# Kernel optimization log

Measured on AMD Instinct MI355X. Metric: run time of the kernel, lower is better.

The kernel has to match this reference:

```python
import jax, jax.numpy as jnp
import numpy as np

B, T, DKQ, DV, EKQ, EV, H, OUT = 8, 2048, 64, 64, 128, 128, 4, 32
FF = 4 * EV
NEG = -1e30  # additive mask value (safe stand-in for -inf)


def _ln(x, g, b, eps=1e-5):
    m = x.mean(-1, keepdims=True)
    var = ((x - m) ** 2).mean(-1, keepdims=True)
    return (x - m) * jax.lax.rsqrt(var + eps) * g + b


def _attn(q, k, v, mask):
    # q,k,v: [n, T, E] -> heads [n, H, T, dh]; NOTE: no 1/sqrt(d) scaling (faithful to source)
    n, t, _ = q.shape
    q = q.reshape(n, t, H, -1).transpose(0, 2, 1, 3)
    k = k.reshape(n, t, H, -1).transpose(0, 2, 1, 3)
    v = v.reshape(n, t, H, -1).transpose(0, 2, 1, 3)
    w = jnp.einsum('bhqd,bhkd->bhqk', q, k) + mask  # [n,H,T,T]
    a = jax.nn.softmax(w, axis=-1)
    o = jnp.einsum('bhqk,bhkd->bhqd', a, v)
    return o.transpose(0, 2, 1, 3).reshape(n, t, -1)


def setup_inputs() -> dict:
    key = jax.random.key(0)
    ks = jax.random.split(key, 32)
    w = lambda k, s: jax.random.normal(k, s, jnp.float32) * 0.02
    DIN_A = DKQ + DV
    return {
        'kq': jax.random.normal(ks[0], (B, T, DKQ), jnp.float32),
        'v': jax.random.normal(ks[1], (B, T, DV), jnp.float32),
        # Layer A (input_dim = DKQ+DV, embed = EV)
        'A_Wk': w(ks[2], (DIN_A, EV)), 'A_bk': jnp.zeros((EV,), jnp.float32),
        'A_Wq': w(ks[3], (DIN_A, EV)), 'A_bq': jnp.zeros((EV,), jnp.float32),
        'A_Wv': w(ks[4], (DIN_A, EV)), 'A_bv': jnp.zeros((EV,), jnp.float32),
        'A_f1W': w(ks[5], (EV, FF)), 'A_f1b': jnp.zeros((FF,), jnp.float32),
        'A_f2W': w(ks[6], (FF, EV)), 'A_f2b': jnp.zeros((EV,), jnp.float32),
        'A_n1g': jnp.ones((EV,), jnp.float32), 'A_n1b': jnp.zeros((EV,), jnp.float32),
        'A_n2g': jnp.ones((EV,), jnp.float32), 'A_n2b': jnp.zeros((EV,), jnp.float32),
        # Layer B (kq -> EKQ, vA -> EV)
        'B_Wk': w(ks[7], (DKQ, EKQ)), 'B_bk': jnp.zeros((EKQ,), jnp.float32),
        'B_Wq': w(ks[8], (DKQ, EKQ)), 'B_bq': jnp.zeros((EKQ,), jnp.float32),
        'B_Wv': w(ks[9], (EV, EV)), 'B_bv': jnp.zeros((EV,), jnp.float32),
        'B_f1W': w(ks[10], (EV, FF)), 'B_f1b': jnp.zeros((FF,), jnp.float32),
        'B_f2W': w(ks[11], (FF, EV)), 'B_f2b': jnp.zeros((EV,), jnp.float32),
        # Output head
        'out_W': w(ks[12], (EV, OUT)), 'out_b': jnp.zeros((OUT,), jnp.float32),
    }


def reference(kq, v, A_Wk, A_bk, A_Wq, A_bq, A_Wv, A_bv, A_f1W, A_f1b, A_f2W, A_f2b,
              A_n1g, A_n1b, A_n2g, A_n2b, B_Wk, B_bk, B_Wq, B_bq, B_Wv, B_bv,
              B_f1W, B_f1b, B_f2W, B_f2b, out_W, out_b):
    n, t, _ = kq.shape
    i = jnp.arange(t)[:, None]
    j = jnp.arange(t)[None, :]
    mask_a = jnp.where(j <= i, 0.0, NEG).astype(jnp.float32)               # causal (diag=1)
    mask_b = jnp.where((j < i) | ((i == 0) & (j == 0)), 0.0, NEG).astype(jnp.float32)  # strict causal + (0,0) exception

    # ---- Layer A ----
    X = jnp.concatenate([kq, v], axis=-1)
    K = X @ A_Wk + A_bk
    Q = X @ A_Wq + A_bq
    V = X @ A_Wv + A_bv
    attn_out = _attn(Q, K, V, mask_a)
    h1 = _ln(V + attn_out, A_n1g, A_n1b)
    ff = jax.nn.gelu(h1 @ A_f1W + A_f1b, approximate=False) @ A_f2W + A_f2b
    vA = _ln(h1 + ff, A_n2g, A_n2b)

    # ---- Layer B (no residuals / norms: values is overwritten in source) ----
    K2 = kq @ B_Wk + B_bk
    Q2 = kq @ B_Wq + B_bq
    V2 = vA @ B_Wv + B_bv
    attn_out2 = _attn(Q2, K2, V2, mask_b)
    ff2 = jax.nn.gelu(attn_out2 @ B_f1W + B_f1b, approximate=False) @ B_f2W + B_f2b

    return ff2 @ out_W + out_b
```

## Files before the change

kernel.cpp:

```cpp
#include <hip/hip_runtime.h>
#include <hip/hip_bf16.h>

#define TSEQ 2048
#define NBATCH 8
#define NROWS (NBATCH*TSEQ)
#define EMB 128
#define NH 4
#define DH 32
#define OUTD 32
#define APLANE (NROWS*EMB)

typedef short s8v __attribute__((ext_vector_type(8)));
typedef float f4v __attribute__((ext_vector_type(4)));

__device__ __forceinline__ unsigned short f2bf(float f){
  unsigned int u = __float_as_uint(f);
  unsigned int r = u + 0x7fffu + ((u >> 16) & 1u);
  return (unsigned short)(r >> 16);
}
__device__ __forceinline__ float bf2f(unsigned short u){
  return __uint_as_float(((unsigned int)u) << 16);
}

struct WPack {
  const float* src[10];
  int off[10];
  int ntk[10];
  int rowoff[10];
  int nsh[10];
  int kn[10];
};
__global__ __launch_bounds__(256) void prep_w(WPack p, short* __restrict__ warena){
  int blk = blockIdx.x, m = 0;
  #pragma unroll
  for (int i=0;i<10;i++){
    int nb = p.kn[i] >> 8;
    if (blk < nb){ m = i; break; }
    blk -= nb;
  }
  int idx = blk*256 + threadIdx.x;
  float x = p.src[m][idx];
  int nsh = p.nsh[m];
  int n = idx & ((1<<nsh)-1);
  int k = idx >> nsh;
  int K = p.kn[m] >> nsh;
  unsigned short hi = f2bf(x);
  unsigned short lo = f2bf(x - bf2f(hi));
  short* dh = warena + p.off[m] + (size_t)(p.rowoff[m] + n)*K + k;
  dh[0]        = (short)hi;
  dh[p.ntk[m]] = (short)lo;
}

__global__ __launch_bounds__(256) void xsplit(const float* __restrict__ kq, const float* __restrict__ v,
                                              unsigned short* __restrict__ X){
  int idx = blockIdx.x*256 + threadIdx.x;
  int row = idx >> 7, c = idx & 127;
  float val = (c < 64) ? kq[row*64 + c] : v[row*64 + (c-64)];
  unsigned short hi = f2bf(val);
  X[idx]          = hi;
  X[idx + APLANE] = f2bf(val - bf2f(hi));
}

struct GOuts {
  const float* bias[3];
  float* of[3];
  unsigned short* ob[3];
};
__global__ __launch_bounds__(256) void gemm2(
    const unsigned short* __restrict__ A, int aplane, int lda, int K, int niter,
    const short* __restrict__ wt, int NTK,
    GOuts og, int NT, int nseg, int act){
  __shared__ short As[2][2][64*40];
  const int tid  = threadIdx.x;
  const int w    = tid >> 6;
  const int lane = tid & 63;
  const int col  = lane & 15;
  const int quad = lane >> 4;
  const int row0 = blockIdx.x * 64;
  const int colg = blockIdx.y*64 + w*16 + col;
  const bool two = (aplane != 0);

  f4v acc[4];
  #pragma unroll
  for (int i=0;i<4;i++) acc[i] = (f4v){0.f,0.f,0.f,0.f};

  const int ar = tid >> 2, ac = (tid & 3)*8;
  const unsigned short* abase = A + (size_t)(row0 + ar)*lda;

  s8v pah, pal;
  pah = *(const s8v*)(abase + ac);
  if (two) pal = *(const s8v*)(abase + aplane + ac);

  for (int i=0;i<niter;i++){
    const int buf = i & 1;
    *(s8v*)&As[buf][0][ar*40 + ac] = pah;
    if (two) *(s8v*)&As[buf][1][ar*40 + ac] = pal;
    __syncthreads();
    if (i+1 < niter){
      const int kcol = (i+1)*32 + ac;
      pah = *(const s8v*)(abase + kcol);
      if (two) pal = *(const s8v*)(abase + aplane + kcol);
    }
    const short* wp = wt + (size_t)colg*K + i*32 + quad*8;
    s8v bh = *(const s8v*)wp;
    s8v bl = *(const s8v*)(wp + NTK);
    #pragma unroll
    for (int rt=0;rt<4;rt++){
      s8v ah = *(const s8v*)&As[buf][0][(rt*16 + col)*40 + quad*8];
      acc[rt] = __builtin_amdgcn_mfma_f32_16x16x32_bf16(ah, bh, acc[rt], 0, 0, 0);
      if (two){
        s8v al = *(const s8v*)&As[buf][1][(rt*16 + col)*40 + quad*8];
        acc[rt] = __builtin_amdgcn_mfma_f32_16x16x32_bf16(al, bh, acc[rt], 0, 0, 0);
      }
      acc[rt] = __builtin_amdgcn_mfma_f32_16x16x32_bf16(ah, bl, acc[rt], 0, 0, 0);
    }
  }

  int seg, lcol, ldc;
  if (nseg > 1){ seg = colg >> 7; lcol = colg & 127; ldc = 128; }
  else         { seg = 0; lcol = colg; ldc = NT; }
  const float bv = og.bias[seg][lcol];
  float* of = og.of[seg];
  unsigned short* ob = og.ob[seg];
  #pragma unroll
  for (int rt=0;rt<4;rt++){
    #pragma unroll
    for (int r=0;r<4;r++){
      const int row = row0 + rt*16 + quad*4 + r;
      float val = acc[rt][r] + bv;
      if (act == 1) val = 0.5f*val*(1.f + erff(val*0.70710678118654752440f));
      if (ob) ob[(size_t)row*ldc + lcol] = f2bf(val);
      else    of[(size_t)row*ldc + lcol] = val;
    }
  }
}

__global__ __launch_bounds__(256) void vtrans(const float* __restrict__ V, unsigned short* __restrict__ Vtb){
  __shared__ short Lt[64*40];
  const int tid = threadIdx.x;
  const int t0 = blockIdx.x * 64;
  const int bh = blockIdx.y;
  const int b = bh >> 2, h = bh & 3;
  {
    const int r = tid >> 2, c = (tid & 3)*8;
    const float* src = V + (size_t)(b*TSEQ + t0 + r)*EMB + h*DH + c;
    float4 x0 = *(const float4*)src;
    float4 x1 = *(const float4*)(src + 4);
    s8v kb;
    kb[0]=(short)f2bf(x0.x); kb[1]=(short)f2bf(x0.y); kb[2]=(short)f2bf(x0.z); kb[3]=(short)f2bf(x0.w);
    kb[4]=(short)f2bf(x1.x); kb[5]=(short)f2bf(x1.y); kb[6]=(short)f2bf(x1.z); kb[7]=(short)f2bf(x1.w);
    *(s8v*)&Lt[r*40 + c] = kb;
  }
  __syncthreads();
  const int d = tid >> 3, kc = (tid & 7)*8;
  s8v o;
  #pragma unroll
  for (int j=0;j<8;j++) o[j] = Lt[(kc + j)*40 + d];
  *(s8v*)(Vtb + ((size_t)bh*32 + d)*TSEQ + t0 + kc) = o;
}

#define KT_STRIDE 40
#define VT_STRIDE 72
#define PW_STRIDE 72
__global__ __launch_bounds__(128) void flash3(const unsigned short* __restrict__ Qb,
                                              const unsigned short* __restrict__ Kb,
                                              const unsigned short* __restrict__ Vtb,
                                              float* __restrict__ O0, float* __restrict__ O1,
                                              float* __restrict__ L0, float* __restrict__ L1,
                                              int mode){
  __shared__ short Kt[64*KT_STRIDE];
  __shared__ short Vt[32*VT_STRIDE];
  __shared__ short Pw[2][16*PW_STRIDE];
  const int tid  = threadIdx.x;
  const int w    = tid >> 6;
  const int lane = tid & 63;
  const int col  = lane & 15;
  const int quad = lane >> 4;
  const int bh = blockIdx.y;
  const int b = bh >> 2, h = bh & 3;
  const int par = blockIdx.z;
  float* Op = par ? O1 : O0;
  float* Lp = par ? L1 : L0;
  const int kr = tid >> 1, kc16 = (tid & 1)*16;
  const int vd = tid >> 2, vk16 = (tid & 3)*16;

  for (int pass = 0; pass < 2; pass++){
    const int t = pass ? blockIdx.x : (63 - blockIdx.x);
    const int qbase = t*32 + w*16;
    const int jtmax = t >> 1;

    s8v qf = *(const s8v*)(Qb + (size_t)(b*TSEQ + qbase + col)*EMB + h*DH + quad*8);
    f4v o0 = {0.f,0.f,0.f,0.f}, o1 = {0.f,0.f,0.f,0.f};
    float lr[4] = {0.f,0.f,0.f,0.f};

    if (par <= jtmax){
      s8v ka, kb2, va, vb;
      {
        const unsigned short* kp = Kb + (size_t)(b*TSEQ + par*64 + kr)*EMB + h*DH + kc16;
        ka = *(const s8v*)kp; kb2 = *(const s8v*)(kp + 8);
        const unsigned short* vp = Vtb + ((size_t)bh*32 + vd)*TSEQ + par*64 + vk16;
        va = *(const s8v*)vp; vb = *(const s8v*)(vp + 8);
      }
      for (int jt = par; jt <= jtmax; jt += 2){
        __syncthreads();
        *(s8v*)&Kt[kr*KT_STRIDE + kc16]     = ka;
        *(s8v*)&Kt[kr*KT_STRIDE + kc16 + 8] = kb2;
        *(s8v*)&Vt[vd*VT_STRIDE + vk16]     = va;
        *(s8v*)&Vt[vd*VT_STRIDE + vk16 + 8] = vb;
        __syncthreads();
        if (jt + 2 <= jtmax){
          const unsigned short* kp = Kb + (size_t)(b*TSEQ + (jt+2)*64 + kr)*EMB + h*DH + kc16;
          ka = *(const s8v*)kp; kb2 = *(const s8v*)(kp + 8);
          const unsigned short* vp = Vtb + ((size_t)bh*32 + vd)*TSEQ + (jt+2)*64 + vk16;
          va = *(const s8v*)vp; vb = *(const s8v*)(vp + 8);
        }
        f4v s[4];
        #pragma unroll
        for (int t4=0;t4<4;t4++){
          s8v kf = *(const s8v*)&Kt[(t4*16 + col)*KT_STRIDE + quad*8];
          f4v z = {0.f,0.f,0.f,0.f};
          s[t4] = __builtin_amdgcn_mfma_f32_16x16x32_bf16(qf, kf, z, 0, 0, 0);
        }
        if (jt == jtmax){
          const int j0 = jt*64;
          #pragma unroll
          for (int t4=0;t4<4;t4++){
            const int jg = j0 + t4*16 + col;
            #pragma unroll
            for (int r=0;r<4;r++){
              const int qg = qbase + quad*4 + r;
              const bool ok = (mode==0) ? (jg <= qg) : ((jg < qg) || (qg==0 && jg==0));
              s[t4][r] = ok ? s[t4][r] : -1e30f;
            }
          }
        }
        #pragma unroll
        for (int t4=0;t4<4;t4++){
          #pragma unroll
          for (int r=0;r<4;r++){
            float pv = __expf(s[t4][r]);
            s[t4][r] = pv;
            lr[r] += pv;
            Pw[w][(quad*4+r)*PW_STRIDE + t4*16 + col] = (short)f2bf(pv);
          }
        }
        #pragma unroll
        for (int kk=0;kk<2;kk++){
          s8v pf  = *(const s8v*)&Pw[w][col*PW_STRIDE + kk*32 + quad*8];
          s8v vf0 = *(const s8v*)&Vt[(col)*VT_STRIDE    + kk*32 + quad*8];
          s8v vf1 = *(const s8v*)&Vt[(16+col)*VT_STRIDE + kk*32 + quad*8];
          o0 = __builtin_amdgcn_mfma_f32_16x16x32_bf16(pf, vf0, o0, 0, 0, 0);
          o1 = __builtin_amdgcn_mfma_f32_16x16x32_bf16(pf, vf1, o1, 0, 0, 0);
        }
      }
    }
    float* obase = Op + (size_t)(b*TSEQ + qbase)*EMB + h*DH;
    #pragma unroll
    for (int r=0;r<4;r++){
      float l = lr[r];
      l += __shfl_xor(l,1); l += __shfl_xor(l,2);
      l += __shfl_xor(l,4); l += __shfl_xor(l,8);
      obase[(size_t)(quad*4+r)*EMB + col]      = o0[r];
      obase[(size_t)(quad*4+r)*EMB + 16 + col] = o1[r];
      if (col == 0) Lp[(size_t)(b*TSEQ + qbase + quad*4 + r)*NH + h] = l;
    }
  }
}

__global__ __launch_bounds__(64) void combine_ln(const float* __restrict__ O0, const float* __restrict__ O1,
                                                 const float* __restrict__ L0, const float* __restrict__ L1,
                                                 const float* __restrict__ Vf,
                                                 const float* __restrict__ g, const float* __restrict__ bt,
                                                 unsigned short* __restrict__ outp){
  const int row = blockIdx.x;
  const int tid = threadIdx.x;
  const size_t base = (size_t)row*EMB;
  const int h0 = tid >> 5, h1i = 2 + (tid >> 5);
  const float la = L0[(size_t)row*NH + h0] + L1[(size_t)row*NH + h0];
  const float lb = L0[(size_t)row*NH + h1i] + L1[(size_t)row*NH + h1i];
  float x0 = Vf[base+tid]    + (O0[base+tid]    + O1[base+tid])    / la;
  float x1 = Vf[base+tid+64] + (O0[base+tid+64] + O1[base+tid+64]) / lb;
  float s  = x0 + x1;
  float s2 = x0*x0 + x1*x1;
  #pragma unroll
  for (int off=1; off<64; off<<=1){
    s  += __shfl_xor(s,  off);
    s2 += __shfl_xor(s2, off);
  }
  float mean = s * (1.f/128.f);
  float var  = s2 * (1.f/128.f) - mean*mean;
  float rstd = rsqrtf(var + 1e-5f);
  float y0 = (x0-mean)*rstd*g[tid]    + bt[tid];
  float y1 = (x1-mean)*rstd*g[tid+64] + bt[tid+64];
  unsigned short h0b = f2bf(y0), h1b = f2bf(y1);
  outp[base+tid]             = h0b;
  outp[base+tid+64]          = h1b;
  outp[base+tid+APLANE]      = f2bf(y0 - bf2f(h0b));
  outp[base+tid+64+APLANE]   = f2bf(y1 - bf2f(h1b));
}

__global__ __launch_bounds__(64) void ln2(const unsigned short* __restrict__ Xp, const float* __restrict__ R,
                                          const float* __restrict__ g, const float* __restrict__ bt,
                                          unsigned short* __restrict__ outp){
  const int row = blockIdx.x;
  const int tid = threadIdx.x;
  const size_t base = (size_t)row*EMB;
  float x0 = bf2f(Xp[base+tid])    + bf2f(Xp[base+tid+APLANE])    + R[base+tid];
  float x1 = bf2f(Xp[base+tid+64]) + bf2f(Xp[base+tid+64+APLANE]) + R[base+tid+64];
  float s  = x0 + x1;
  float s2 = x0*x0 + x1*x1;
  #pragma unroll
  for (int off=1; off<64; off<<=1){
    s  += __shfl_xor(s,  off);
    s2 += __shfl_xor(s2, off);
  }
  float mean = s * (1.f/128.f);
  float var  = s2 * (1.f/128.f) - mean*mean;
  float rstd = rsqrtf(var + 1e-5f);
  float y0 = (x0-mean)*rstd*g[tid]    + bt[tid];
  float y1 = (x1-mean)*rstd*g[tid+64] + bt[tid+64];
  unsigned short h0b = f2bf(y0), h1b = f2bf(y1);
  outp[base+tid]             = h0b;
  outp[base+tid+64]          = h1b;
  outp[base+tid+APLANE]      = f2bf(y0 - bf2f(h0b));
  outp[base+tid+64+APLANE]   = f2bf(y1 - bf2f(h1b));
}

__global__ __launch_bounds__(256) void combine_b(const float* __restrict__ O0, const float* __restrict__ O1,
                                                 const float* __restrict__ L0, const float* __restrict__ L1,
                                                 unsigned short* __restrict__ outp){
  const int idx = blockIdx.x*256 + threadIdx.x;
  const int row = idx >> 7, c = idx & 127, h = c >> 5;
  const float l = L0[(size_t)row*NH + h] + L1[(size_t)row*NH + h];
  const float v = (O0[idx] + O1[idx]) / l;
  unsigned short hb = f2bf(v);
  outp[idx]          = hb;
  outp[idx + APLANE] = f2bf(v - bf2f(hb));
}

__global__ __launch_bounds__(256) void out_proj(const float* __restrict__ A,
                                                const float* __restrict__ W, const float* __restrict__ bb,
                                                float* __restrict__ out){
  __shared__ float As[8*128];
  __shared__ float Ws2[128*32];
  const int tid = threadIdx.x;
  const int row0 = blockIdx.x * 8;
  for (int idx = tid; idx < 8*128; idx += 256) As[idx] = A[(size_t)row0*128 + idx];
  for (int idx = tid; idx < 128*32; idx += 256) Ws2[idx] = W[idx];
  __syncthreads();
  const int r = tid >> 5, c = tid & 31;
  float acc = bb[c];
  #pragma unroll 8
  for (int k=0;k<128;k++) acc = fmaf(As[r*128 + k], Ws2[k*32 + c], acc);
  out[(size_t)(row0 + r)*OUTD + c] = acc;
}

extern "C" void kernel_launch(void* const* d_in, const int* in_sizes, int n_in,
                              void* d_out, int out_size, void* d_ws, size_t ws_size,
                              hipStream_t stream) {
  const float* kq    = (const float*)d_in[0];
  const float* v     = (const float*)d_in[1];
  const float* A_Wk  = (const float*)d_in[2];  const float* A_bk  = (const float*)d_in[3];
  const float* A_Wq  = (const float*)d_in[4];  const float* A_bq  = (const float*)d_in[5];
  const float* A_Wv  = (const float*)d_in[6];  const float* A_bv  = (const float*)d_in[7];
  const float* A_f1W = (const float*)d_in[8];  const float* A_f1b = (const float*)d_in[9];
  const float* A_f2W = (const float*)d_in[10]; const float* A_f2b = (const float*)d_in[11];
  const float* A_n1g = (const float*)d_in[12]; const float* A_n1b = (const float*)d_in[13];
  const float* A_n2g = (const float*)d_in[14]; const float* A_n2b = (const float*)d_in[15];
  const float* B_Wk  = (const float*)d_in[16]; const float* B_bk  = (const float*)d_in[17];
  const float* B_Wq  = (const float*)d_in[18]; const float* B_bq  = (const float*)d_in[19];
  const float* B_Wv  = (const float*)d_in[20]; const float* B_bv  = (const float*)d_in[21];
  const float* B_f1W = (const float*)d_in[22]; const float* B_f1b = (const float*)d_in[23];
  const float* B_f2W = (const float*)d_in[24]; const float* B_f2b = (const float*)d_in[25];
  const float* out_W = (const float*)d_in[26]; const float* out_b = (const float*)d_in[27];
  float* out = (float*)d_out;
  (void)in_sizes; (void)n_in; (void)out_size; (void)ws_size;

  char* ws = (char*)d_ws;
  const size_t MB = 1024*1024;
  short* warena = (short*)ws;
  unsigned short* Xs  = (unsigned short*)(ws + 2*MB);
  unsigned short* Qbf = (unsigned short*)(ws + 10*MB);
  unsigned short* Kbf = (unsigned short*)(ws + 14*MB);
  unsigned short* Vtb = (unsigned short*)(ws + 18*MB);
  float* Vf  = (float*)(ws + 22*MB);
  float* O0  = (float*)(ws + 30*MB);
  float* O1  = (float*)(ws + 38*MB);
  float* L0  = (float*)(ws + 46*MB);
  float* L1  = (float*)(ws + 47*MB);
  unsigned short* h1p = (unsigned short*)(ws + 48*MB);
  unsigned short* mid = (unsigned short*)(ws + 56*MB);
  float* ffo = (float*)(ws + 72*MB);
  unsigned short* vAp = (unsigned short*)(ws + 80*MB);

  WPack p;
  const float* srcs[10] = {A_Wq,A_Wk,A_Wv,A_f1W,A_f2W,B_Wq,B_Wk,B_Wv,B_f1W,B_f2W};
  int kn[10]     = {16384,16384,16384,65536,65536,8192,8192,16384,65536,65536};
  int nsh[10]    = {7,7,7,9,7,7,7,7,9,7};
  int off[10]    = {0,0,0,98304,229376,360448,360448,393216,425984,557056};
  int ntk[10]    = {49152,49152,49152,65536,65536,16384,16384,16384,65536,65536};
  int rowoff[10] = {0,128,256,0,0,0,128,0,0,0};
  int nblk = 0;
  for (int i=0;i<10;i++){
    p.src[i]=srcs[i]; p.kn[i]=kn[i]; p.nsh[i]=nsh[i];
    p.off[i]=off[i]; p.ntk[i]=ntk[i]; p.rowoff[i]=rowoff[i];
    nblk += kn[i] >> 8;
  }
  prep_w<<<nblk, 256, 0, stream>>>(p, warena);
  xsplit<<<NROWS*128/256, 256, 0, stream>>>(kq, v, Xs);

  GOuts oQKVA = {{A_bq,A_bk,A_bv},{nullptr,nullptr,Vf},{Qbf,Kbf,nullptr}};
  GOuts oF1A  = {{A_f1b,nullptr,nullptr},{nullptr,nullptr,nullptr},{mid,nullptr,nullptr}};
  GOuts oF2A  = {{A_f2b,nullptr,nullptr},{ffo,nullptr,nullptr},{nullptr,nullptr,nullptr}};
  GOuts oQKB  = {{B_bq,B_bk,nullptr},{nullptr,nullptr,nullptr},{Qbf,Kbf,nullptr}};
  GOuts oVB   = {{B_bv,nullptr,nullptr},{Vf,nullptr,nullptr},{nullptr,nullptr,nullptr}};
  GOuts oF1B  = {{B_f1b,nullptr,nullptr},{nullptr,nullptr,nullptr},{mid,nullptr,nullptr}};
  GOuts oF2B  = {{B_f2b,nullptr,nullptr},{ffo,nullptr,nullptr},{nullptr,nullptr,nullptr}};

  gemm2<<<dim3(256,6), 256, 0, stream>>>(Xs, APLANE, 128, 128, 4, warena + 0,      49152, oQKVA, 384, 3, 0);
  vtrans<<<dim3(32,32), 256, 0, stream>>>(Vf, Vtb);
  flash3<<<dim3(32,32,2), 128, 0, stream>>>(Qbf, Kbf, Vtb, O0, O1, L0, L1, 0);
  combine_ln<<<NROWS, 64, 0, stream>>>(O0, O1, L0, L1, Vf, A_n1g, A_n1b, h1p);
  gemm2<<<dim3(256,8), 256, 0, stream>>>(h1p, APLANE, 128, 128, 4, warena + 98304, 65536, oF1A, 512, 1, 1);
  gemm2<<<dim3(256,2), 256, 0, stream>>>(mid, 0,      512, 512, 16, warena + 229376, 65536, oF2A, 128, 1, 0);
  ln2<<<NROWS, 64, 0, stream>>>(h1p, ffo, A_n2g, A_n2b, vAp);

  gemm2<<<dim3(256,4), 256, 0, stream>>>(Xs, APLANE, 128, 64, 2,  warena + 360448, 16384, oQKB, 256, 2, 0);
  gemm2<<<dim3(256,2), 256, 0, stream>>>(vAp, APLANE, 128, 128, 4, warena + 393216, 16384, oVB, 128, 1, 0);
  vtrans<<<dim3(32,32), 256, 0, stream>>>(Vf, Vtb);
  flash3<<<dim3(32,32,2), 128, 0, stream>>>(Qbf, Kbf, Vtb, O0, O1, L0, L1, 1);
  combine_b<<<NROWS*128/256, 256, 0, stream>>>(O0, O1, L0, L1, h1p);
  gemm2<<<dim3(256,8), 256, 0, stream>>>(h1p, APLANE, 128, 128, 4, warena + 425984, 65536, oF1B, 512, 1, 1);
  gemm2<<<dim3(256,2), 256, 0, stream>>>(mid, 0,      512, 512, 16, warena + 557056, 65536, oF2B, 128, 1, 0);

  out_proj<<<NROWS/8, 256, 0, stream>>>(ffo, out_W, out_b, out);
}
```

Baseline: 313.5 us.

## Fold FFN2 into output head, fuse V transpose into GEMM, swap flash operands

Several changes at once. B_f2W and out_W are pre-multiplied into one 512x32 matrix, so the last FFN2 GEMM and the output projection become a single small kernel reading the bf16 GELU activations. The V-transpose kernels are removed because the QKV/V GEMM epilogue now writes the transposed bf16 V directly. Q is prescaled by log2e so flash uses exp2. The flash MFMA operands are swapped so results are laid out per query row, allowing vectorized stores and a simpler row-sum reduction. The GEMM also prefetches B fragments a step ahead. The weight folding changes rounding order, and out2 is a plain FMA loop over K=512 per output, which may be slower than the MFMA GEMM it replaces.

```diff
diff --git a/kernel.cpp b/kernel.cpp
--- a/kernel.cpp
+++ b/kernel.cpp
@@ -9,8 +9,10 @@
 #define DH 32
 #define OUTD 32
 #define APLANE (NROWS*EMB)
+#define LOG2E 1.4426950408889634f
 
 typedef short s8v __attribute__((ext_vector_type(8)));
+typedef short s4v __attribute__((ext_vector_type(4)));
 typedef float f4v __attribute__((ext_vector_type(4)));
 
 __device__ __forceinline__ unsigned short f2bf(float f){
@@ -51,6 +53,24 @@
   dh[p.ntk[m]] = (short)lo;
 }
 
+__global__ __launch_bounds__(256) void prep_wc(const float* __restrict__ f2W, const float* __restrict__ f2b,
+                                               const float* __restrict__ oW, const float* __restrict__ ob,
+                                               float* __restrict__ Wc, float* __restrict__ bc){
+  int idx = blockIdx.x*256 + threadIdx.x;
+  if (idx < 512*32){
+    int k = idx >> 5, n = idx & 31;
+    float s = 0.f;
+    #pragma unroll 4
+    for (int j=0;j<128;j++) s = fmaf(f2W[k*128+j], oW[j*32+n], s);
+    Wc[idx] = s;
+  } else if (idx < 512*32 + 32){
+    int n = idx - 512*32;
+    float s = ob[n];
+    for (int j=0;j<128;j++) s = fmaf(f2b[j], oW[j*32+n], s);
+    bc[n] = s;
+  }
+}
+
 __global__ __launch_bounds__(256) void xsplit(const float* __restrict__ kq, const float* __restrict__ v,
                                               unsigned short* __restrict__ X){
   int idx = blockIdx.x*256 + threadIdx.x;
@@ -65,6 +85,8 @@
   const float* bias[3];
   float* of[3];
   unsigned short* ob[3];
+  unsigned short* vt[3];
+  float scale[3];
 };
 __global__ __launch_bounds__(256) void gemm2(
     const unsigned short* __restrict__ A, int aplane, int lda, int K, int niter,
@@ -86,24 +108,27 @@
 
   const int ar = tid >> 2, ac = (tid & 3)*8;
   const unsigned short* abase = A + (size_t)(row0 + ar)*lda;
-
-  s8v pah, pal;
+  const short* wbase = wt + (size_t)colg*K + quad*8;
+
+  s8v pah, pal, pbh, pbl;
   pah = *(const s8v*)(abase + ac);
   if (two) pal = *(const s8v*)(abase + aplane + ac);
+  pbh = *(const s8v*)(wbase);
+  pbl = *(const s8v*)(wbase + NTK);
 
   for (int i=0;i<niter;i++){
     const int buf = i & 1;
     *(s8v*)&As[buf][0][ar*40 + ac] = pah;
     if (two) *(s8v*)&As[buf][1][ar*40 + ac] = pal;
     __syncthreads();
+    s8v bh = pbh, bl = pbl;
     if (i+1 < niter){
-      const int kcol = (i+1)*32 + ac;
-      pah = *(const s8v*)(abase + kcol);
-      if (two) pal = *(const s8v*)(abase + aplane + kcol);
-    }
-    const short* wp = wt + (size_t)colg*K + i*32 + quad*8;
-    s8v bh = *(const s8v*)wp;
-    s8v bl = *(const s8v*)(wp + NTK);
+      const int kcol = (i+1)*32;
+      pah = *(const s8v*)(abase + kcol + ac);
+      if (two) pal = *(const s8v*)(abase + aplane + kcol + ac);
+      pbh = *(const s8v*)(wbase + kcol);
+      pbl = *(const s8v*)(wbase + NTK + kcol);
+    }
     #pragma unroll
     for (int rt=0;rt<4;rt++){
       s8v ah = *(const s8v*)&As[buf][0][(rt*16 + col)*40 + quad*8];
@@ -120,43 +145,41 @@
   if (nseg > 1){ seg = colg >> 7; lcol = colg & 127; ldc = 128; }
   else         { seg = 0; lcol = colg; ldc = NT; }
   const float bv = og.bias[seg][lcol];
+  const float sc = og.scale[seg];
   float* of = og.of[seg];
   unsigned short* ob = og.ob[seg];
+  unsigned short* vtp = og.vt[seg];
+  float vals[4][4];
   #pragma unroll
   for (int rt=0;rt<4;rt++){
     #pragma unroll
     for (int r=0;r<4;r++){
-      const int row = row0 + rt*16 + quad*4 + r;
       float val = acc[rt][r] + bv;
       if (act == 1) val = 0.5f*val*(1.f + erff(val*0.70710678118654752440f));
-      if (ob) ob[(size_t)row*ldc + lcol] = f2bf(val);
-      else    of[(size_t)row*ldc + lcol] = val;
-    }
-  }
-}
-
-__global__ __launch_bounds__(256) void vtrans(const float* __restrict__ V, unsigned short* __restrict__ Vtb){
-  __shared__ short Lt[64*40];
-  const int tid = threadIdx.x;
-  const int t0 = blockIdx.x * 64;
-  const int bh = blockIdx.y;
-  const int b = bh >> 2, h = bh & 3;
-  {
-    const int r = tid >> 2, c = (tid & 3)*8;
-    const float* src = V + (size_t)(b*TSEQ + t0 + r)*EMB + h*DH + c;
-    float4 x0 = *(const float4*)src;
-    float4 x1 = *(const float4*)(src + 4);
-    s8v kb;
-    kb[0]=(short)f2bf(x0.x); kb[1]=(short)f2bf(x0.y); kb[2]=(short)f2bf(x0.z); kb[3]=(short)f2bf(x0.w);
-    kb[4]=(short)f2bf(x1.x); kb[5]=(short)f2bf(x1.y); kb[6]=(short)f2bf(x1.z); kb[7]=(short)f2bf(x1.w);
-    *(s8v*)&Lt[r*40 + c] = kb;
-  }
-  __syncthreads();
-  const int d = tid >> 3, kc = (tid & 7)*8;
-  s8v o;
-  #pragma unroll
-  for (int j=0;j<8;j++) o[j] = Lt[(kc + j)*40 + d];
-  *(s8v*)(Vtb + ((size_t)bh*32 + d)*TSEQ + t0 + kc) = o;
+      vals[rt][r] = val * sc;
+    }
+  }
+  #pragma unroll
+  for (int rt=0;rt<4;rt++){
+    const int row = row0 + rt*16 + quad*4;
+    #pragma unroll
+    for (int r=0;r<4;r++){
+      if (ob)      ob[(size_t)(row+r)*ldc + lcol] = f2bf(vals[rt][r]);
+      else if (of) of[(size_t)(row+r)*ldc + lcol] = vals[rt][r];
+    }
+  }
+  if (vtp){
+    const int hh = lcol >> 5, dd = lcol & 31;
+    const int bb = row0 >> 11;
+    unsigned short* vbase = vtp + ((size_t)(bb*NH + hh)*32 + dd)*TSEQ + (row0 & (TSEQ-1)) + quad*4;
+    #pragma unroll
+    for (int rt=0;rt<4;rt++){
+      s4v pk;
+      #pragma unroll
+      for (int r=0;r<4;r++) pk[r] = (short)f2bf(vals[rt][r]);
+      *(s4v*)(vbase + rt*16) = pk;
+    }
+  }
 }
 
 #define KT_STRIDE 40
@@ -188,10 +211,11 @@
     const int t = pass ? blockIdx.x : (63 - blockIdx.x);
     const int qbase = t*32 + w*16;
     const int jtmax = t >> 1;
-
-    s8v qf = *(const s8v*)(Qb + (size_t)(b*TSEQ + qbase + col)*EMB + h*DH + quad*8);
+    const int qg = qbase + col;
+
+    s8v qf = *(const s8v*)(Qb + (size_t)(b*TSEQ + qg)*EMB + h*DH + quad*8);
     f4v o0 = {0.f,0.f,0.f,0.f}, o1 = {0.f,0.f,0.f,0.f};
-    float lr[4] = {0.f,0.f,0.f,0.f};
+    float lsum = 0.f;
 
     if (par <= jtmax){
       s8v ka, kb2, va, vb;
@@ -219,16 +243,15 @@
         for (int t4=0;t4<4;t4++){
           s8v kf = *(const s8v*)&Kt[(t4*16 + col)*KT_STRIDE + quad*8];
           f4v z = {0.f,0.f,0.f,0.f};
-          s[t4] = __builtin_amdgcn_mfma_f32_16x16x32_bf16(qf, kf, z, 0, 0, 0);
+          s[t4] = __builtin_amdgcn_mfma_f32_16x16x32_bf16(kf, qf, z, 0, 0, 0);
         }
         if (jt == jtmax){
           const int j0 = jt*64;
           #pragma unroll
           for (int t4=0;t4<4;t4++){
-            const int jg = j0 + t4*16 + col;
             #pragma unroll
             for (int r=0;r<4;r++){
-              const int qg = qbase + quad*4 + r;
+              const int jg = j0 + t4*16 + quad*4 + r;
               const bool ok = (mode==0) ? (jg <= qg) : ((jg < qg) || (qg==0 && jg==0));
               s[t4][r] = ok ? s[t4][r] : -1e30f;
             }
@@ -236,34 +259,31 @@
         }
         #pragma unroll
         for (int t4=0;t4<4;t4++){
+          s4v pk;
           #pragma unroll
           for (int r=0;r<4;r++){
-            float pv = __expf(s[t4][r]);
-            s[t4][r] = pv;
-            lr[r] += pv;
-            Pw[w][(quad*4+r)*PW_STRIDE + t4*16 + col] = (short)f2bf(pv);
+            float pv = exp2f(s[t4][r]);
+            lsum += pv;
+            pk[r] = (short)f2bf(pv);
           }
+          *(s4v*)&Pw[w][col*PW_STRIDE + t4*16 + quad*4] = pk;
         }
         #pragma unroll
         for (int kk=0;kk<2;kk++){
           s8v pf  = *(const s8v*)&Pw[w][col*PW_STRIDE + kk*32 + quad*8];
           s8v vf0 = *(const s8v*)&Vt[(col)*VT_STRIDE    + kk*32 + quad*8];
           s8v vf1 = *(const s8v*)&Vt[(16+col)*VT_STRIDE + kk*32 + quad*8];
-          o0 = __builtin_amdgcn_mfma_f32_16x16x32_bf16(pf, vf0, o0, 0, 0, 0);
-          o1 = __builtin_amdgcn_mfma_f32_16x16x32_bf16(pf, vf1, o1, 0, 0, 0);
+          o0 = __builtin_amdgcn_mfma_f32_16x16x32_bf16(vf0, pf, o0, 0, 0, 0);
+          o1 = __builtin_amdgcn_mfma_f32_16x16x32_bf16(vf1, pf, o1, 0, 0, 0);
         }
       }
     }
-    float* obase = Op + (size_t)(b*TSEQ + qbase)*EMB + h*DH;
-    #pragma unroll
-    for (int r=0;r<4;r++){
-      float l = lr[r];
-      l += __shfl_xor(l,1); l += __shfl_xor(l,2);
-      l += __shfl_xor(l,4); l += __shfl_xor(l,8);
-      obase[(size_t)(quad*4+r)*EMB + col]      = o0[r];
-      obase[(size_t)(quad*4+r)*EMB + 16 + col] = o1[r];
-      if (col == 0) Lp[(size_t)(b*TSEQ + qbase + quad*4 + r)*NH + h] = l;
-    }
+    lsum += __shfl_xor(lsum, 16);
+    lsum += __shfl_xor(lsum, 32);
+    float* obase = Op + (size_t)(b*TSEQ + qg)*EMB + h*DH + quad*4;
+    *(float4*)(obase)      = make_float4(o0[0],o0[1],o0[2],o0[3]);
+    *(float4*)(obase + 16) = make_float4(o1[0],o1[1],o1[2],o1[3]);
+    if (quad == 0) Lp[(size_t)(b*TSEQ + qg)*NH + h] = lsum;
   }
 }
 
@@ -338,21 +358,21 @@
   outp[idx + APLANE] = f2bf(v - bf2f(hb));
 }
 
-__global__ __launch_bounds__(256) void out_proj(const float* __restrict__ A,
-                                                const float* __restrict__ W, const float* __restrict__ bb,
-                                                float* __restrict__ out){
-  __shared__ float As[8*128];
-  __shared__ float Ws2[128*32];
+__global__ __launch_bounds__(256) void out2(const unsigned short* __restrict__ mid,
+                                            const float* __restrict__ Wc, const float* __restrict__ bc,
+                                            float* __restrict__ out){
+  __shared__ float As[8*512];
   const int tid = threadIdx.x;
-  const int row0 = blockIdx.x * 8;
-  for (int idx = tid; idx < 8*128; idx += 256) As[idx] = A[(size_t)row0*128 + idx];
-  for (int idx = tid; idx < 128*32; idx += 256) Ws2[idx] = W[idx];
+  const int row0 = blockIdx.x*8;
+  for (int idx = tid; idx < 8*512; idx += 256)
+    As[idx] = bf2f(mid[(size_t)row0*512 + idx]);
   __syncthreads();
   const int r = tid >> 5, c = tid & 31;
-  float acc = bb[c];
+  float acc = bc[c];
+  const float* as = &As[r*512];
   #pragma unroll 8
-  for (int k=0;k<128;k++) acc = fmaf(As[r*128 + k], Ws2[k*32 + c], acc);
-  out[(size_t)(row0 + r)*OUTD + c] = acc;
+  for (int k=0;k<512;k++) acc = fmaf(as[k], Wc[k*32+c], acc);
+  out[(size_t)(row0+r)*OUTD + c] = acc;
 }
 
 extern "C" void kernel_launch(void* const* d_in, const int* in_sizes, int n_in,
@@ -379,6 +399,8 @@
   char* ws = (char*)d_ws;
   const size_t MB = 1024*1024;
   short* warena = (short*)ws;
+  float* Wc  = (float*)(ws + 1536*1024);
+  float* bc  = (float*)(ws + 1536*1024 + 65536);
   unsigned short* Xs  = (unsigned short*)(ws + 2*MB);
   unsigned short* Qbf = (unsigned short*)(ws + 10*MB);
   unsigned short* Kbf = (unsigned short*)(ws + 14*MB);
@@ -407,18 +429,17 @@
     nblk += kn[i] >> 8;
   }
   prep_w<<<nblk, 256, 0, stream>>>(p, warena);
+  prep_wc<<<65, 256, 0, stream>>>(B_f2W, B_f2b, out_W, out_b, Wc, bc);
   xsplit<<<NROWS*128/256, 256, 0, stream>>>(kq, v, Xs);
 
-  GOuts oQKVA = {{A_bq,A_bk,A_bv},{nullptr,nullptr,Vf},{Qbf,Kbf,nullptr}};
-  GOuts oF1A  = {{A_f1b,nullptr,nullptr},{nullptr,nullptr,nullptr},{mid,nullptr,nullptr}};
-  GOuts oF2A  = {{A_f2b,nullptr,nullptr},{ffo,nullptr,nullptr},{nullptr,nullptr,nullptr}};
-  GOuts oQKB  = {{B_bq,B_bk,nullptr},{nullptr,nullptr,nullptr},{Qbf,Kbf,nullptr}};
-  GOuts oVB   = {{B_bv,nullptr,nullptr},{Vf,nullptr,nullptr},{nullptr,nullptr,nullptr}};
-  GOuts oF1B  = {{B_f1b,nullptr,nullptr},{nullptr,nullptr,nullptr},{mid,nullptr,nullptr}};
-  GOuts oF2B  = {{B_f2b,nullptr,nullptr},{ffo,nullptr,nullptr},{nullptr,nullptr,nullptr}};
+  GOuts oQKVA = {{A_bq,A_bk,A_bv},{nullptr,nullptr,Vf},{Qbf,Kbf,nullptr},{nullptr,nullptr,Vtb},{LOG2E,1.f,1.f}};
+  GOuts oF1A  = {{A_f1b,nullptr,nullptr},{nullptr,nullptr,nullptr},{mid,nullptr,nullptr},{nullptr,nullptr,nullptr},{1.f,1.f,1.f}};
+  GOuts oF2A  = {{A_f2b,nullptr,nullptr},{ffo,nullptr,nullptr},{nullptr,nullptr,nullptr},{nullptr,nullptr,nullptr},{1.f,1.f,1.f}};
+  GOuts oQKB  = {{B_bq,B_bk,nullptr},{nullptr,nullptr,nullptr},{Qbf,Kbf,nullptr},{nullptr,nullptr,nullptr},{LOG2E,1.f,1.f}};
+  GOuts oVB   = {{B_bv,nullptr,nullptr},{nullptr,nullptr,nullptr},{nullptr,nullptr,nullptr},{Vtb,nullptr,nullptr},{1.f,1.f,1.f}};
+  GOuts oF1B  = {{B_f1b,nullptr,nullptr},{nullptr,nullptr,nullptr},{mid,nullptr,nullptr},{nullptr,nullptr,nullptr},{1.f,1.f,1.f}};
 
   gemm2<<<dim3(256,6), 256, 0, stream>>>(Xs, APLANE, 128, 128, 4, warena + 0,      49152, oQKVA, 384, 3, 0);
-  vtrans<<<dim3(32,32), 256, 0, stream>>>(Vf, Vtb);
   flash3<<<dim3(32,32,2), 128, 0, stream>>>(Qbf, Kbf, Vtb, O0, O1, L0, L1, 0);
   combine_ln<<<NROWS, 64, 0, stream>>>(O0, O1, L0, L1, Vf, A_n1g, A_n1b, h1p);
   gemm2<<<dim3(256,8), 256, 0, stream>>>(h1p, APLANE, 128, 128, 4, warena + 98304, 65536, oF1A, 512, 1, 1);
@@ -427,11 +448,8 @@
 
   gemm2<<<dim3(256,4), 256, 0, stream>>>(Xs, APLANE, 128, 64, 2,  warena + 360448, 16384, oQKB, 256, 2, 0);
   gemm2<<<dim3(256,2), 256, 0, stream>>>(vAp, APLANE, 128, 128, 4, warena + 393216, 16384, oVB, 128, 1, 0);
-  vtrans<<<dim3(32,32), 256, 0, stream>>>(Vf, Vtb);
   flash3<<<dim3(32,32,2), 128, 0, stream>>>(Qbf, Kbf, Vtb, O0, O1, L0, L1, 1);
   combine_b<<<NROWS*128/256, 256, 0, stream>>>(O0, O1, L0, L1, h1p);
   gemm2<<<dim3(256,8), 256, 0, stream>>>(h1p, APLANE, 128, 128, 4, warena + 425984, 65536, oF1B, 512, 1, 1);
-  gemm2<<<dim3(256,2), 256, 0, stream>>>(mid, 0,      512, 512, 16, warena + 557056, 65536, oF2B, 128, 1, 0);
-
-  out_proj<<<NROWS/8, 256, 0, stream>>>(ffo, out_W, out_b, out);
-}
+  out2<<<NROWS/8, 256, 0, stream>>>(mid, Wc, bc, out);
+}
```

Measured after the change: 333.1 us. 6.3% more time.
